# Performance work log

Hardware: AMD Instinct MI355X
Metric: run time of the kernel (lower is better)

## Reference

```python
import jax, jax.numpy as jnp
import numpy as np

B, H, S, D = 2, 12, 1024, 128
KQ, KK = 6, 11  # per-head conv kernel over (query, key) score plane


def setup_inputs() -> dict:
    key = jax.random.key(0)
    kq, kk, kv, kw = jax.random.split(key, 4)
    Q = jax.random.normal(kq, (B, H, S, D), dtype=jnp.float32)
    K = jax.random.normal(kk, (B, H, S, D), dtype=jnp.float32)
    V = jax.random.normal(kv, (B, H, S, D), dtype=jnp.float32)
    W = jax.random.normal(kw, (H, KQ, KK), dtype=jnp.float32) * 0.1
    return {"Q": Q, "K": K, "V": V, "W": W}


def reference(Q, K, V, W):
    # causal=True, softmax_scale = 1/sqrt(head_dim)  (module defaults)
    b, h, s, d = Q.shape
    _, kq, kk = W.shape
    pad_q = kq - 1            # causal padding along the query axis
    pad_k = (kk - 1) // 2     # 'same' padding along the key axis
    scale = 1.0 / np.sqrt(d).astype(np.float32)

    # Raw QK^T scores: [b, h, s_q, s_k]
    scores = jnp.einsum('bhqd,bhkd->bhqk', Q, K)

    # Causal: zero out future keys before the conv so the kernel cannot mix
    # in future information (matches the `causal` flag passed into the
    # fused qk_conv kernel; out-of-range tiles load as 0 in the Triton code).
    tril = jnp.tril(jnp.ones((s, s), dtype=bool))
    scores = jnp.where(tril[None, None], scores, 0.0)

    # Per-head 2D conv over the (q, k) plane: grouped conv with H groups,
    # kernel W[h] applied to head h's score map. Cross-correlation (PyTorch
    # conv semantics == lax.conv_general_dilated without kernel flip).
    conv = jax.lax.conv_general_dilated(
        scores,                      # [b, h, s, s] as NCHW
        W[:, None, :, :],            # [h, 1, kq, kk] as OIHW, groups=h
        window_strides=(1, 1),
        padding=((pad_q, 0), (pad_k, pad_k)),
        feature_group_count=h,
        dimension_numbers=('NCHW', 'OIHW', 'NCHW'),
    )

    # Scale, re-apply causal mask with the kernel's -1e6 fill, softmax, @V.
    logits = conv * scale + jnp.where(tril[None, None], 0.0, -1000000.0)
    P = jax.nn.softmax(logits, axis=-1)
    O = jnp.einsum('bhqk,bhkd->bhqd', P, V)
    return O
```

## Files before the change

### kernel.cpp

```cpp
#include <hip/hip_runtime.h>
#include <hip/hip_bf16.h>
#include <math.h>

#define B_ 2
#define H_ 12
#define S_ 1024
#define D_ 128
#define BH_ (B_ * H_)
#define SCALE 0.08838834764831843f

#define QPAD 16
#define QROWS (S_ + QPAD)

#define NB_KH   768
#define NB_QP   3120
#define NB_VT   3072
#define NB_PREPA (NB_KH + NB_QP + NB_VT)

typedef __attribute__((ext_vector_type(8))) short short8;
typedef __attribute__((ext_vector_type(4))) float floatx4;

__device__ __forceinline__ unsigned short f2b(float f) {
    return __builtin_bit_cast(unsigned short, __float2bfloat16(f));
}

__global__ __launch_bounds__(256) void prep_a_kernel(
    const float* __restrict__ Q, const float* __restrict__ K,
    const float* __restrict__ V, const float* __restrict__ W,
    unsigned short* __restrict__ Qp, unsigned short* __restrict__ KhF,
    unsigned short* __restrict__ VhF)
{
    __shared__ __align__(16) union {
        float kld[42][132];
        float vt_ls[32][33];
    } sm;
    const int blk = blockIdx.x;
    const int tid = threadIdx.x;

    if (blk < NB_KH) {
        const int bh = blk >> 5, kt = blk & 31;
        const int h = bh % H_;
        const int k0 = kt * 32;
        for (int p = tid; p < 42 * 32; p += 256) {
            const int r = p >> 5, c4 = (p & 31) * 4;
            const int gk = k0 - 5 + r;
            float4 v = make_float4(0.f, 0.f, 0.f, 0.f);
            if (gk >= 0 && gk < S_)
                v = *(const float4*)(K + ((size_t)bh * S_ + gk) * D_ + c4);
            *(float4*)&sm.kld[r][c4] = v;
        }
        __syncthreads();
        const int wv = tid >> 6, ln = tid & 63;
        const float* Wh = W + h * 66;
        const size_t obase = (size_t)blk * 24576;
        #pragma unroll
        for (int nt = 0; nt < 2; ++nt) {
            const int lr = nt * 16 + (ln & 15);
            const int d0 = wv * 32 + (ln >> 4) * 8;
            float a[6][8];
            #pragma unroll
            for (int i = 0; i < 6; ++i)
                #pragma unroll
                for (int e = 0; e < 8; ++e) a[i][e] = 0.f;
            #pragma unroll
            for (int j = 0; j < 11; ++j) {
                const float4 v0 = *(const float4*)&sm.kld[lr + j][d0];
                const float4 v1 = *(const float4*)&sm.kld[lr + j][d0 + 4];
                #pragma unroll
                for (int i = 0; i < 6; ++i) {
                    const float w = Wh[i * 11 + j];
                    a[i][0] += w * v0.x; a[i][1] += w * v0.y;
                    a[i][2] += w * v0.z; a[i][3] += w * v0.w;
                    a[i][4] += w * v1.x; a[i][5] += w * v1.y;
                    a[i][6] += w * v1.z; a[i][7] += w * v1.w;
                }
            }
            #pragma unroll
            for (int i = 0; i < 6; ++i) {
                short8 o;
                #pragma unroll
                for (int e = 0; e < 8; ++e) o[e] = (short)f2b(a[i][e] * SCALE);
                *(short8*)(KhF + obase + (size_t)(((i * 4 + wv) * 2 + nt) * 64 + ln) * 8) = o;
            }
        }
    } else if (blk < NB_KH + NB_QP) {
        const int idx = (blk - NB_KH) * 256 + tid;
        const size_t e0 = (size_t)idx * 4;
        const int bh = (int)(e0 / ((size_t)QROWS * D_));
        const int rem = (int)(e0 - (size_t)bh * QROWS * D_);
        const int r = rem / D_;
        const int d = rem - r * D_;
        const int sr = r - QPAD;
        float4 v = make_float4(0.f, 0.f, 0.f, 0.f);
        if (sr >= 0 && sr < S_)
            v = *(const float4*)(Q + ((size_t)bh * S_ + sr) * D_ + d);
        ushort4 o; o.x = f2b(v.x); o.y = f2b(v.y); o.z = f2b(v.z); o.w = f2b(v.w);
        *(ushort4*)(Qp + ((size_t)bh * QROWS + r) * D_ + d) = o;
    } else {
        const int b2 = blk - (NB_KH + NB_QP);
        const int dt = b2 & 3, ktl = (b2 >> 2) & 31, bh = b2 >> 7;
        const int lk = tid >> 3, ld = (tid & 7) * 4;
        const float4 v4 = *(const float4*)(V + ((size_t)bh * S_ + ktl * 32 + lk) * D_ + dt * 32 + ld);
        sm.vt_ls[lk][ld + 0] = v4.x; sm.vt_ls[lk][ld + 1] = v4.y;
        sm.vt_ls[lk][ld + 2] = v4.z; sm.vt_ls[lk][ld + 3] = v4.w;
        __syncthreads();
        const int lk2 = tid >> 3, lc = (tid & 7) * 4;
        const int pb = ((lc >> 3) << 2) | (((lc >> 2) & 1) << 4);
        const int d = dt * 32 + lk2;
        const int nd = d >> 4, l15v = d & 15;
        ushort4 o;
        o.x = f2b(sm.vt_ls[pb + 0][lk2]); o.y = f2b(sm.vt_ls[pb + 1][lk2]);
        o.z = f2b(sm.vt_ls[pb + 2][lk2]); o.w = f2b(sm.vt_ls[pb + 3][lk2]);
        const size_t addr = ((size_t)((bh * 32 + ktl) * 8 + nd) * 64
                             + (lc >> 3) * 16 + l15v) * 8 + (lc & 7);
        *(ushort4*)(VhF + addr) = o;
    }
}

__global__ __launch_bounds__(256) void prep_corr_kernel(
    const float* __restrict__ Q, const float* __restrict__ K,
    const float* __restrict__ W, float* __restrict__ Corr)
{
    __shared__ __align__(16) struct {
        float Qs[69][132];
        float Ks[78][132];
        float band[69][16];
    } sm;
    const int cb = blockIdx.x;
    const int tid = threadIdx.x;
    const int bh = cb >> 4, q0c = (cb & 15) * 64;
    const int h = bh % H_;

    for (int p = tid; p < 69 * 32; p += 256) {
        const int r = p >> 5, c4 = (p & 31) * 4;
        const int gq = q0c - 5 + r;
        float4 v = make_float4(0.f, 0.f, 0.f, 0.f);
        if (gq >= 0 && gq < S_)
            v = *(const float4*)(Q + ((size_t)bh * S_ + gq) * D_ + c4);
        *(float4*)&sm.Qs[r][c4] = v;
    }
    for (int p = tid; p < 78 * 32; p += 256) {
        const int r = p >> 5, c4 = (p & 31) * 4;
        const int gk = q0c - 4 + r;
        float4 v = make_float4(0.f, 0.f, 0.f, 0.f);
        if (gk >= 0 && gk < S_)
            v = *(const float4*)(K + ((size_t)bh * S_ + gk) * D_ + c4);
        *(float4*)&sm.Ks[r][c4] = v;
    }
    __syncthreads();
    for (int s = tid; s < 69 * 16; s += 256) {
        const int r = s >> 4, dsl = s & 15;
        float v = 0.f;
        if (dsl < 10) {
            const float4* qr = (const float4*)&sm.Qs[r][0];
            const float4* kr = (const float4*)&sm.Ks[r + dsl][0];
            #pragma unroll 8
            for (int c = 0; c < 32; ++c) {
                const float4 a = qr[c], b = kr[c];
                v += a.x * b.x + a.y * b.y + a.z * b.z + a.w * b.w;
            }
        }
        sm.band[r][dsl] = v;
    }
    __syncthreads();
    for (int e = tid; e < 64 * 16; e += 256) {
        const int ql = e >> 4, d = e & 15;
        float v = 0.f;
        if (d <= 10) {
            for (int i2 = 0; i2 < 6; ++i2)
                for (int j = i2 + d + 1; j < 11; ++j)
                    v += W[h * 66 + i2 * 11 + j] * SCALE * sm.band[ql + i2][j - i2 - d - 1];
        }
        Corr[((size_t)bh << 14) + ((size_t)(q0c + ql) << 4) + d] = v;
    }
}

__global__ __launch_bounds__(256, 2) void conv_attn_mfma(
    const unsigned short* __restrict__ Qp,
    const unsigned short* __restrict__ KhF,
    const unsigned short* __restrict__ VhF,
    const float* __restrict__ Corr,
    float* __restrict__ O,
    float* __restrict__ Op1,
    float* __restrict__ L0, float* __restrict__ L1)
{
    const int tid = threadIdx.x;
    const int wv = tid >> 6;
    const int ln = tid & 63;
    const int l15 = ln & 15;
    const int qd = ln >> 4;

    const int bid = blockIdx.x;
    const int slot = bid >> 3;
    const int bh = (bid & 7) * 3 + slot / 20;
    const int r20 = slot % 20;
    const int r = r20 >> 1;
    const int half = r20 & 1;

    const unsigned short* Khb = KhF + (size_t)(bh * 32) * 24576 + ln * 8;
    const unsigned short* Vhb = VhF + (size_t)(bh * 32) * 4096 + ln * 8;
    const float* Cb = Corr + ((size_t)bh << 14);

    const int nit = (r < 6) ? 2 : 1;
    for (int item = 0; item < nit; ++item) {
        int qb, ks;
        if (r < 6) { ks = r & 1; qb = (item == 0) ? (r >> 1) : (5 - (r >> 1)); }
        else       { ks = r & 1; qb = 6 + ((r - 6) >> 1); }

        const int wl = half * 4 + wv;
        const int qw0 = qb * 128 + wl * 16;
        const int ktw = 4 * qb + (wl >> 1);
        const int klo = ks * (2 * qb + 2);
        const int ntile = 2 * qb + 2;

        short8 qf[6][4];
        {
            const unsigned short* qbase =
                Qp + ((size_t)bh * QROWS + qw0 + 11 + l15) * D_ + qd * 8;
            #pragma unroll
            for (int i = 0; i < 6; ++i)
                #pragma unroll
                for (int kc = 0; kc < 4; ++kc)
                    qf[i][kc] = *(const short8*)(qbase + (size_t)i * D_ + kc * 32);
        }

        floatx4 acc[8];
        #pragma unroll
        for (int nd = 0; nd < 8; ++nd) acc[nd] = (floatx4){0.f, 0.f, 0.f, 0.f};
        float l_run = 0.f;

        for (int t = 0; t < ntile; ++t) {
            const int kt = klo + t;
            if (kt > ktw) break;
            const int k0 = kt * 32;
            const unsigned short* A = Khb + (size_t)kt * 24576;

            short8 vf[8];
            #pragma unroll
            for (int nd = 0; nd < 8; ++nd)
                vf[nd] = *(const short8*)(Vhb + (size_t)kt * 4096 + nd * 512);

            floatx4 s0 = {0.f, 0.f, 0.f, 0.f}, s1 = {0.f, 0.f, 0.f, 0.f};
            #pragma unroll
            for (int c = 0; c < 24; ++c) {
                const short8 a0 = *(const short8*)(A + c * 1024);
                const short8 a1 = *(const short8*)(A + c * 1024 + 512);
                const short8 b = qf[c >> 2][c & 3];
                s0 = __builtin_amdgcn_mfma_f32_16x16x32_bf16(a0, b, s0, 0, 0, 0);
                s1 = __builtin_amdgcn_mfma_f32_16x16x32_bf16(a1, b, s1, 0, 0, 0);
            }

            const bool need_corr = (kt >= ktw - 1);
            const int qrow = qw0 + l15;
            float sum = 0.f;
            short8 pbv;
            #pragma unroll
            for (int nt = 0; nt < 2; ++nt)
                #pragma unroll
                for (int rg = 0; rg < 4; ++rg) {
                    const int kcol = k0 + nt * 16 + qd * 4 + rg;
                    float v = nt ? s1[rg] : s0[rg];
                    if (need_corr) {
                        const int dd = qrow - kcol;
                        if (dd >= 0 && dd <= 10) v -= Cb[(qrow << 4) + dd];
                    }
                    const float p = (kcol <= qrow) ? __expf(v) : 0.f;
                    sum += p;
                    pbv[nt * 4 + rg] = (short)f2b(p);
                }
            sum += __shfl_xor(sum, 16);
            sum += __shfl_xor(sum, 32);
            l_run += sum;

            #pragma unroll
            for (int nd = 0; nd < 8; ++nd)
                acc[nd] = __builtin_amdgcn_mfma_f32_16x16x32_bf16(pbv, vf[nd], acc[nd], 0, 0, 0);
        }

        float* Ob = ks ? Op1 : O;
        float* Lb = ks ? L1 : L0;
        if (qd == 0) Lb[bh * S_ + qw0 + l15] = l_run;
        #pragma unroll
        for (int rg = 0; rg < 4; ++rg) {
            const int row = qw0 + qd * 4 + rg;
            float* orow = Ob + ((size_t)bh * S_ + row) * D_;
            #pragma unroll
            for (int nd = 0; nd < 8; ++nd)
                orow[nd * 16 + l15] = acc[nd][rg];
        }
    }
}

__global__ __launch_bounds__(256) void merge_kernel(
    float* __restrict__ O, const float* __restrict__ Op1,
    const float* __restrict__ L0, const float* __restrict__ L1)
{
    const int idx = blockIdx.x * 256 + threadIdx.x;
    const int row = idx >> 5;
    const float inv = 1.f / (L0[row] + L1[row]);
    const float4 a = ((const float4*)O)[idx];
    const float4 b = ((const float4*)Op1)[idx];
    float4 o;
    o.x = (a.x + b.x) * inv; o.y = (a.y + b.y) * inv;
    o.z = (a.z + b.z) * inv; o.w = (a.w + b.w) * inv;
    ((float4*)O)[idx] = o;
}

extern "C" void kernel_launch(void* const* d_in, const int* in_sizes, int n_in,
                              void* d_out, int out_size, void* d_ws, size_t ws_size,
                              hipStream_t stream) {
    const float* Q = (const float*)d_in[0];
    const float* K = (const float*)d_in[1];
    const float* V = (const float*)d_in[2];
    const float* W = (const float*)d_in[3];
    float* O = (float*)d_out;

    unsigned short* Qp  = (unsigned short*)d_ws;
    unsigned short* KhF = (unsigned short*)((char*)d_ws + 6389760);
    unsigned short* VhF = (unsigned short*)((char*)d_ws + 44138496);
    float*          Cr  = (float*)((char*)d_ws + 50429952);
    float*          Op1 = (float*)((char*)d_ws + 52002816);
    float*          L0  = (float*)((char*)d_ws + 64585728);
    float*          L1  = (float*)((char*)d_ws + 64684032);

    prep_a_kernel<<<dim3(NB_PREPA), dim3(256), 0, stream>>>(Q, K, V, W, Qp, KhF, VhF);
    prep_corr_kernel<<<dim3(384), dim3(256), 0, stream>>>(Q, K, W, Cr);
    conv_attn_mfma<<<dim3(480), dim3(256), 0, stream>>>(Qp, KhF, VhF, Cr, O, Op1, L0, L1);
    merge_kernel<<<dim3(3072), dim3(256), 0, stream>>>(O, Op1, L0, L1);
}
```

Baseline: 209.5 us.

## Split attention key range four ways with finer per-wave work distribution

The main attention kernel now gives each wave its own 16-row query strip and splits that strip's key tiles into four nearly equal chunks. Grid grows from 480 to 1536 blocks and launch bounds rise to 3 blocks per CU, aiming for better load balance across the causal triangle and higher occupancy. The price is two more partial output buffers and more merge traffic, with the merge kernel now summing four partials. The correction prep kernel also reads Q straight from global memory instead of staging it in shared memory, which cuts LDS use and adds bounds checks.

```diff
diff --git a/kernel.cpp b/kernel.cpp
--- a/kernel.cpp
+++ b/kernel.cpp
@@ -122,7 +122,6 @@
     const float* __restrict__ W, float* __restrict__ Corr)
 {
     __shared__ __align__(16) struct {
-        float Qs[69][132];
         float Ks[78][132];
         float band[69][16];
     } sm;
@@ -131,14 +130,6 @@
     const int bh = cb >> 4, q0c = (cb & 15) * 64;
     const int h = bh % H_;
 
-    for (int p = tid; p < 69 * 32; p += 256) {
-        const int r = p >> 5, c4 = (p & 31) * 4;
-        const int gq = q0c - 5 + r;
-        float4 v = make_float4(0.f, 0.f, 0.f, 0.f);
-        if (gq >= 0 && gq < S_)
-            v = *(const float4*)(Q + ((size_t)bh * S_ + gq) * D_ + c4);
-        *(float4*)&sm.Qs[r][c4] = v;
-    }
     for (int p = tid; p < 78 * 32; p += 256) {
         const int r = p >> 5, c4 = (p & 31) * 4;
         const int gk = q0c - 4 + r;
@@ -151,8 +142,9 @@
     for (int s = tid; s < 69 * 16; s += 256) {
         const int r = s >> 4, dsl = s & 15;
         float v = 0.f;
-        if (dsl < 10) {
-            const float4* qr = (const float4*)&sm.Qs[r][0];
+        const int qp = q0c - 5 + r;
+        if (dsl < 10 && qp >= 0 && qp + dsl + 1 < S_) {
+            const float4* qr = (const float4*)(Q + ((size_t)bh * S_ + qp) * D_);
             const float4* kr = (const float4*)&sm.Ks[r + dsl][0];
             #pragma unroll 8
             for (int c = 0; c < 32; ++c) {
@@ -175,14 +167,15 @@
     }
 }
 
-__global__ __launch_bounds__(256, 2) void conv_attn_mfma(
+__global__ __launch_bounds__(256, 3) void conv_attn_mfma(
     const unsigned short* __restrict__ Qp,
     const unsigned short* __restrict__ KhF,
     const unsigned short* __restrict__ VhF,
     const float* __restrict__ Corr,
     float* __restrict__ O,
-    float* __restrict__ Op1,
-    float* __restrict__ L0, float* __restrict__ L1)
+    float* __restrict__ Op1, float* __restrict__ Op2, float* __restrict__ Op3,
+    float* __restrict__ L0, float* __restrict__ L1,
+    float* __restrict__ L2, float* __restrict__ L3)
 {
     const int tid = threadIdx.x;
     const int wv = tid >> 6;
@@ -191,118 +184,120 @@
     const int qd = ln >> 4;
 
     const int bid = blockIdx.x;
+    const int xcd = bid & 7;
     const int slot = bid >> 3;
-    const int bh = (bid & 7) * 3 + slot / 20;
-    const int r20 = slot % 20;
-    const int r = r20 >> 1;
-    const int half = r20 & 1;
+    const int bh = xcd * 3 + slot / 64;
+    const int inner = slot & 63;
+    const int sg = 15 - (inner >> 2);
+    const int ks = inner & 3;
+
+    const int s = sg * 4 + wv;
+    const int qw0 = s * 16;
+    const int ktw = s >> 1;
+    const int n = ktw + 1;
+    const int qtr = n >> 2, rem = n & 3;
+    const int cnt = qtr + (ks < rem ? 1 : 0);
+    const int klo = ks * qtr + (ks < rem ? ks : rem);
 
     const unsigned short* Khb = KhF + (size_t)(bh * 32) * 24576 + ln * 8;
     const unsigned short* Vhb = VhF + (size_t)(bh * 32) * 4096 + ln * 8;
     const float* Cb = Corr + ((size_t)bh << 14);
 
-    const int nit = (r < 6) ? 2 : 1;
-    for (int item = 0; item < nit; ++item) {
-        int qb, ks;
-        if (r < 6) { ks = r & 1; qb = (item == 0) ? (r >> 1) : (5 - (r >> 1)); }
-        else       { ks = r & 1; qb = 6 + ((r - 6) >> 1); }
-
-        const int wl = half * 4 + wv;
-        const int qw0 = qb * 128 + wl * 16;
-        const int ktw = 4 * qb + (wl >> 1);
-        const int klo = ks * (2 * qb + 2);
-        const int ntile = 2 * qb + 2;
-
-        short8 qf[6][4];
-        {
-            const unsigned short* qbase =
-                Qp + ((size_t)bh * QROWS + qw0 + 11 + l15) * D_ + qd * 8;
-            #pragma unroll
-            for (int i = 0; i < 6; ++i)
-                #pragma unroll
-                for (int kc = 0; kc < 4; ++kc)
-                    qf[i][kc] = *(const short8*)(qbase + (size_t)i * D_ + kc * 32);
-        }
-
-        floatx4 acc[8];
-        #pragma unroll
-        for (int nd = 0; nd < 8; ++nd) acc[nd] = (floatx4){0.f, 0.f, 0.f, 0.f};
-        float l_run = 0.f;
-
-        for (int t = 0; t < ntile; ++t) {
-            const int kt = klo + t;
-            if (kt > ktw) break;
-            const int k0 = kt * 32;
-            const unsigned short* A = Khb + (size_t)kt * 24576;
-
-            short8 vf[8];
-            #pragma unroll
-            for (int nd = 0; nd < 8; ++nd)
-                vf[nd] = *(const short8*)(Vhb + (size_t)kt * 4096 + nd * 512);
-
-            floatx4 s0 = {0.f, 0.f, 0.f, 0.f}, s1 = {0.f, 0.f, 0.f, 0.f};
-            #pragma unroll
-            for (int c = 0; c < 24; ++c) {
-                const short8 a0 = *(const short8*)(A + c * 1024);
-                const short8 a1 = *(const short8*)(A + c * 1024 + 512);
-                const short8 b = qf[c >> 2][c & 3];
-                s0 = __builtin_amdgcn_mfma_f32_16x16x32_bf16(a0, b, s0, 0, 0, 0);
-                s1 = __builtin_amdgcn_mfma_f32_16x16x32_bf16(a1, b, s1, 0, 0, 0);
+    short8 qf[6][4];
+    {
+        const unsigned short* qbase =
+            Qp + ((size_t)bh * QROWS + qw0 + 11 + l15) * D_ + qd * 8;
+        #pragma unroll
+        for (int i = 0; i < 6; ++i)
+            #pragma unroll
+            for (int kc = 0; kc < 4; ++kc)
+                qf[i][kc] = *(const short8*)(qbase + (size_t)i * D_ + kc * 32);
+    }
+
+    floatx4 acc[8];
+    #pragma unroll
+    for (int nd = 0; nd < 8; ++nd) acc[nd] = (floatx4){0.f, 0.f, 0.f, 0.f};
+    float l_run = 0.f;
+
+    for (int t = 0; t < cnt; ++t) {
+        const int kt = klo + t;
+        const int k0 = kt * 32;
+        const unsigned short* A = Khb + (size_t)kt * 24576;
+
+        short8 vf[8];
+        #pragma unroll
+        for (int nd = 0; nd < 8; ++nd)
+            vf[nd] = *(const short8*)(Vhb + (size_t)kt * 4096 + nd * 512);
+
+        floatx4 s0 = {0.f, 0.f, 0.f, 0.f}, s1 = {0.f, 0.f, 0.f, 0.f};
+        #pragma unroll
+        for (int c = 0; c < 24; ++c) {
+            const short8 a0 = *(const short8*)(A + c * 1024);
+            const short8 a1 = *(const short8*)(A + c * 1024 + 512);
+            const short8 b = qf[c >> 2][c & 3];
+            s0 = __builtin_amdgcn_mfma_f32_16x16x32_bf16(a0, b, s0, 0, 0, 0);
+            s1 = __builtin_amdgcn_mfma_f32_16x16x32_bf16(a1, b, s1, 0, 0, 0);
+        }
+
+        const bool need_corr = (kt >= ktw - 1);
+        const int qrow = qw0 + l15;
+        float sum = 0.f;
+        short8 pbv;
+        #pragma unroll
+        for (int nt = 0; nt < 2; ++nt)
+            #pragma unroll
+            for (int rg = 0; rg < 4; ++rg) {
+                const int kcol = k0 + nt * 16 + qd * 4 + rg;
+                float v = nt ? s1[rg] : s0[rg];
+                if (need_corr) {
+                    const int dd = qrow - kcol;
+                    if (dd >= 0 && dd <= 10) v -= Cb[(qrow << 4) + dd];
+                }
+                const float p = (kcol <= qrow) ? __expf(v) : 0.f;
+                sum += p;
+                pbv[nt * 4 + rg] = (short)f2b(p);
             }
-
-            const bool need_corr = (kt >= ktw - 1);
-            const int qrow = qw0 + l15;
-            float sum = 0.f;
-            short8 pbv;
-            #pragma unroll
-            for (int nt = 0; nt < 2; ++nt)
-                #pragma unroll
-                for (int rg = 0; rg < 4; ++rg) {
-                    const int kcol = k0 + nt * 16 + qd * 4 + rg;
-                    float v = nt ? s1[rg] : s0[rg];
-                    if (need_corr) {
-                        const int dd = qrow - kcol;
-                        if (dd >= 0 && dd <= 10) v -= Cb[(qrow << 4) + dd];
-                    }
-                    const float p = (kcol <= qrow) ? __expf(v) : 0.f;
-                    sum += p;
-                    pbv[nt * 4 + rg] = (short)f2b(p);
-                }
-            sum += __shfl_xor(sum, 16);
-            sum += __shfl_xor(sum, 32);
-            l_run += sum;
-
-            #pragma unroll
-            for (int nd = 0; nd < 8; ++nd)
-                acc[nd] = __builtin_amdgcn_mfma_f32_16x16x32_bf16(pbv, vf[nd], acc[nd], 0, 0, 0);
-        }
-
-        float* Ob = ks ? Op1 : O;
-        float* Lb = ks ? L1 : L0;
-        if (qd == 0) Lb[bh * S_ + qw0 + l15] = l_run;
-        #pragma unroll
-        for (int rg = 0; rg < 4; ++rg) {
-            const int row = qw0 + qd * 4 + rg;
-            float* orow = Ob + ((size_t)bh * S_ + row) * D_;
-            #pragma unroll
-            for (int nd = 0; nd < 8; ++nd)
-                orow[nd * 16 + l15] = acc[nd][rg];
-        }
+        sum += __shfl_xor(sum, 16);
+        sum += __shfl_xor(sum, 32);
+        l_run += sum;
+
+        #pragma unroll
+        for (int nd = 0; nd < 8; ++nd)
+            acc[nd] = __builtin_amdgcn_mfma_f32_16x16x32_bf16(pbv, vf[nd], acc[nd], 0, 0, 0);
+    }
+
+    float* Ob = (ks == 0) ? O : (ks == 1) ? Op1 : (ks == 2) ? Op2 : Op3;
+    float* Lb = (ks == 0) ? L0 : (ks == 1) ? L1 : (ks == 2) ? L2 : L3;
+    if (qd == 0) Lb[bh * S_ + qw0 + l15] = l_run;
+    #pragma unroll
+    for (int rg = 0; rg < 4; ++rg) {
+        const int row = qw0 + qd * 4 + rg;
+        float* orow = Ob + ((size_t)bh * S_ + row) * D_;
+        #pragma unroll
+        for (int nd = 0; nd < 8; ++nd)
+            orow[nd * 16 + l15] = acc[nd][rg];
     }
 }
 
 __global__ __launch_bounds__(256) void merge_kernel(
-    float* __restrict__ O, const float* __restrict__ Op1,
-    const float* __restrict__ L0, const float* __restrict__ L1)
+    float* __restrict__ O,
+    const float* __restrict__ Op1, const float* __restrict__ Op2,
+    const float* __restrict__ Op3,
+    const float* __restrict__ L0, const float* __restrict__ L1,
+    const float* __restrict__ L2, const float* __restrict__ L3)
 {
     const int idx = blockIdx.x * 256 + threadIdx.x;
     const int row = idx >> 5;
-    const float inv = 1.f / (L0[row] + L1[row]);
+    const float inv = 1.f / (L0[row] + L1[row] + L2[row] + L3[row]);
     const float4 a = ((const float4*)O)[idx];
     const float4 b = ((const float4*)Op1)[idx];
+    const float4 c = ((const float4*)Op2)[idx];
+    const float4 d = ((const float4*)Op3)[idx];
     float4 o;
-    o.x = (a.x + b.x) * inv; o.y = (a.y + b.y) * inv;
-    o.z = (a.z + b.z) * inv; o.w = (a.w + b.w) * inv;
+    o.x = (a.x + b.x + c.x + d.x) * inv;
+    o.y = (a.y + b.y + c.y + d.y) * inv;
+    o.z = (a.z + b.z + c.z + d.z) * inv;
+    o.w = (a.w + b.w + c.w + d.w) * inv;
     ((float4*)O)[idx] = o;
 }
 
@@ -320,11 +315,16 @@
     unsigned short* VhF = (unsigned short*)((char*)d_ws + 44138496);
     float*          Cr  = (float*)((char*)d_ws + 50429952);
     float*          Op1 = (float*)((char*)d_ws + 52002816);
-    float*          L0  = (float*)((char*)d_ws + 64585728);
-    float*          L1  = (float*)((char*)d_ws + 64684032);
+    float*          Op2 = (float*)((char*)d_ws + 64585728);
+    float*          Op3 = (float*)((char*)d_ws + 77168640);
+    float*          L0  = (float*)((char*)d_ws + 89751552);
+    float*          L1  = (float*)((char*)d_ws + 89849856);
+    float*          L2  = (float*)((char*)d_ws + 89948160);
+    float*          L3  = (float*)((char*)d_ws + 90046464);
 
     prep_a_kernel<<<dim3(NB_PREPA), dim3(256), 0, stream>>>(Q, K, V, W, Qp, KhF, VhF);
     prep_corr_kernel<<<dim3(384), dim3(256), 0, stream>>>(Q, K, W, Cr);
-    conv_attn_mfma<<<dim3(480), dim3(256), 0, stream>>>(Qp, KhF, VhF, Cr, O, Op1, L0, L1);
-    merge_kernel<<<dim3(3072), dim3(256), 0, stream>>>(O, Op1, L0, L1);
-}
+    conv_attn_mfma<<<dim3(1536), dim3(256), 0, stream>>>(Qp, KhF, VhF, Cr, O,
+                                                         Op1, Op2, Op3, L0, L1, L2, L3);
+    merge_kernel<<<dim3(3072), dim3(256), 0, stream>>>(O, Op1, Op2, Op3, L0, L1, L2, L3);
+}
```

Measured after the change: 249.8 us. +19.3%, slower.
